# Performance work log

Hardware: AMD Instinct MI355X
Metric: run time of the kernel (lower is better)

## Reference

```python
import jax, jax.numpy as jnp
import numpy as np

N_NODES = 200000
N_EDGES = 1600000
N_GRAPHS = 2000
IN_DIM, W1_DIM, W2_DIM, N_CLASSES = 8, 64, 12, 2


def setup_inputs() -> dict:
    key = jax.random.key(0)
    ks = jax.random.split(key, 9)
    x = jax.random.normal(ks[0], (N_NODES, IN_DIM), dtype=jnp.float32)
    edge_index = jax.random.randint(ks[1], (2, N_EDGES), 0, N_NODES, dtype=jnp.int64)
    batch_index = jnp.sort(jax.random.randint(ks[2], (N_NODES,), 0, N_GRAPHS, dtype=jnp.int64))
    # Glorot-ish scaled params
    W1 = jax.random.normal(ks[3], (IN_DIM, W1_DIM), dtype=jnp.float32) * (1.0 / np.sqrt(IN_DIM))
    b1 = jnp.zeros((W1_DIM,), dtype=jnp.float32)
    W2 = jax.random.normal(ks[4], (W1_DIM, W2_DIM), dtype=jnp.float32) * (1.0 / np.sqrt(W1_DIM))
    b2 = jnp.zeros((W2_DIM,), dtype=jnp.float32)
    Wl = jax.random.normal(ks[5], (W2_DIM, N_CLASSES), dtype=jnp.float32) * (1.0 / np.sqrt(W2_DIM))
    bl = jnp.zeros((N_CLASSES,), dtype=jnp.float32)
    return {"x": x, "edge_index": edge_index, "batch_index": batch_index,
            "W1": W1, "b1": b1, "W2": W2, "b2": b2, "Wl": Wl, "bl": bl}


def _gcn_conv(x, W, b, src, dst, deg_inv_sqrt, n_nodes):
    # x' = D^{-1/2} (A + I) D^{-1/2} X W + b  (self-loops already in src/dst)
    xw = x @ W                                   # [N, out]
    norm = deg_inv_sqrt[src] * deg_inv_sqrt[dst]  # [E+N]
    msg = xw[src] * norm[:, None]                 # edge-wise gather (memory-bound)
    out = jax.ops.segment_sum(msg, dst, num_segments=n_nodes)
    return out + b


def reference(x, edge_index, batch_index, W1, b1, W2, b2, Wl, bl):
    n = x.shape[0]
    loops = jnp.arange(n, dtype=edge_index.dtype)
    src = jnp.concatenate([edge_index[0], loops])
    dst = jnp.concatenate([edge_index[1], loops])
    # degree (with self-loops) on destination nodes, as in PyG gcn_norm
    deg = jax.ops.segment_sum(jnp.ones_like(dst, dtype=x.dtype), dst, num_segments=n)
    deg_inv_sqrt = jax.lax.rsqrt(deg)  # deg >= 1 due to self-loops
    h = jax.nn.relu(_gcn_conv(x, W1, b1, src, dst, deg_inv_sqrt, n))
    h = jax.nn.relu(_gcn_conv(h, W2, b2, src, dst, deg_inv_sqrt, n))
    pooled = jax.ops.segment_max(h, batch_index, num_segments=N_GRAPHS)  # global_max_pool
    logits = pooled @ Wl + bl
    return jax.nn.log_softmax(logits, axis=1)
```

## Files before the change

### kernel.cpp

```cpp
#include <hip/hip_runtime.h>
#include <hip/hip_fp16.h>
#include <stdint.h>


constexpr int IN_DIM = 8;
constexpr int H1 = 64;
constexpr int H2 = 12;
constexpr int NPB = 512;
constexpr int NBK = 391;
constexpr int CAP = 4608;
constexpr int CHUNK = 4096;
constexpr int SLOTS = 16;

typedef float nfloat4 __attribute__((ext_vector_type(4)));
__device__ __forceinline__ void nt_store_f4(void* p, float4 v) {
    nfloat4 w = {v.x, v.y, v.z, v.w};
    __builtin_nontemporal_store(w, (nfloat4*)p);
}

__device__ __forceinline__ void acc_row8(float* acc, int4 rv) {
    const __half2* h = (const __half2*)&rv;
#pragma unroll
    for (int q = 0; q < 4; ++q) {
        float2 f = __half22float2(h[q]);
        acc[2 * q] += f.x; acc[2 * q + 1] += f.y;
    }
}

__global__ void k_binA(const int* __restrict__ src, const int* __restrict__ dst,
                       uint32_t* __restrict__ pairs, int* __restrict__ bcursor, int ne) {
    __shared__ int s_cur[NBK];
    __shared__ int s_gb[NBK];
    for (int i = threadIdx.x; i < NBK; i += 256) s_cur[i] = 0;
    __syncthreads();
    int e0 = blockIdx.x * CHUNK;
    int rec[16];
#pragma unroll
    for (int i = 0; i < 16; ++i) {
        int e = e0 + i * 256 + threadIdx.x;
        rec[i] = -1;
        if (e < ne) {
            int d = __builtin_nontemporal_load(&dst[e]);
            int b = d >> 9;
            int off = atomicAdd(&s_cur[b], 1);
            rec[i] = (off << 18) | ((d & 511) << 9) | b;
        }
    }
    __syncthreads();
    for (int b = threadIdx.x; b < NBK; b += 256) {
        int c = s_cur[b];
        s_gb[b] = (c > 0) ? atomicAdd(&bcursor[b], c) : 0;
    }
    __syncthreads();
#pragma unroll
    for (int i = 0; i < 16; ++i) {
        if (rec[i] < 0) continue;
        int e = e0 + i * 256 + threadIdx.x;
        int b = rec[i] & 511;
        int dl = (rec[i] >> 9) & 511;
        int off = (rec[i] >> 18) + s_gb[b];
        if (off < CAP)
            pairs[(size_t)b * CAP + off] =
                ((uint32_t)dl << 18) | (uint32_t)__builtin_nontemporal_load(&src[e]);
    }
}

__global__ void __launch_bounds__(256) k_binB(
        const uint32_t* __restrict__ pairs, const int* __restrict__ bcursor,
        const float* __restrict__ x, int* __restrict__ csr_pad,
        int* __restrict__ csr_ovf, unsigned int* __restrict__ meta,
        float* __restrict__ dis, __half2* __restrict__ xdh, int n) {
    __shared__ int s_hist[NPB];
    __shared__ int s_start[NPB];
    __shared__ int s_cur[NPB];
    __shared__ int s_tmp[256];
    __shared__ int s_pad[NPB * SLOTS];
    int b = blockIdx.x;
    int t = threadIdx.x;
    int cnt = min(bcursor[b], CAP);
    const uint32_t* pb = pairs + (size_t)b * CAP;
    for (int i = t; i < NPB; i += 256) { s_hist[i] = 0; s_cur[i] = 0; }
    for (int i = t; i < NPB * SLOTS; i += 256) s_pad[i] = n;
    __syncthreads();
    for (int i = t; i < cnt; i += 256)
        atomicAdd(&s_hist[__builtin_nontemporal_load(&pb[i]) >> 18], 1);
    __syncthreads();
    int b2i = t * 2;
    int v0 = s_hist[b2i], v1 = s_hist[b2i + 1];
    int tot = v0 + v1;
    s_tmp[t] = tot;
    __syncthreads();
    for (int off = 1; off < 256; off <<= 1) {
        int u = (t >= off) ? s_tmp[t - off] : 0;
        __syncthreads();
        s_tmp[t] += u;
        __syncthreads();
    }
    int ex = s_tmp[t] - tot;
    s_start[b2i] = ex;
    s_start[b2i + 1] = ex + v0;
    __syncthreads();
    int cb = b * CAP;
    int node0 = b << 9;
    for (int i = t; i < NPB; i += 256) {
        int node = node0 + i;
        if (node < n) {
            meta[node] = ((unsigned int)s_hist[i] << 21) | (unsigned int)(cb + s_start[i]);
            float di = rsqrtf((float)(s_hist[i] + 1));
            dis[node] = di;
            const float4* xi = (const float4*)(x + (size_t)node * IN_DIM);
            float4 a = xi[0], c = xi[1];
            union { __half2 h[4]; int iv[4]; } u;
            u.h[0] = __float22half2_rn(make_float2(a.x * di, a.y * di));
            u.h[1] = __float22half2_rn(make_float2(a.z * di, a.w * di));
            u.h[2] = __float22half2_rn(make_float2(c.x * di, c.y * di));
            u.h[3] = __float22half2_rn(make_float2(c.z * di, c.w * di));
            ((int4*)xdh)[node] = make_int4(u.iv[0], u.iv[1], u.iv[2], u.iv[3]);
        } else if (node == n) {
            ((int4*)xdh)[n] = make_int4(0, 0, 0, 0);
        }
    }
    __syncthreads();
    for (int i = t; i < cnt; i += 256) {
        uint32_t p = __builtin_nontemporal_load(&pb[i]);
        int dl = p >> 18;
        int sidx = (int)(p & 0x3FFFFu);
        int pos = atomicAdd(&s_cur[dl], 1);
        if (pos < SLOTS) s_pad[dl * SLOTS + pos] = sidx;
        else             csr_ovf[cb + s_start[dl] + pos] = sidx;
    }
    __syncthreads();
    for (int i = t; i < NPB * SLOTS / 4; i += 256) {
        int node = node0 + (i >> 2);
        if (node < n)
            ((int4*)csr_pad)[(size_t)node0 * 4 + i] = ((int4*)s_pad)[i];
    }
}

__global__ void __launch_bounds__(256) k_agg1f(
        const int* __restrict__ csr_pad, const int* __restrict__ csr_ovf,
        const unsigned int* __restrict__ meta, const __half2* __restrict__ xdh,
        const float* __restrict__ dis, const float* __restrict__ W1,
        const float* __restrict__ b1, const float* __restrict__ W2,
        __half2* __restrict__ y2h, int n) {
    __shared__ float sW1[IN_DIM * H1];
    __shared__ float sW2[H1 * H2];
    __shared__ float sb1[H1];
    for (int i = threadIdx.x; i < IN_DIM * H1; i += 256) sW1[i] = W1[i];
    for (int i = threadIdx.x; i < H1 * H2; i += 256) sW2[i] = W2[i];
    if (threadIdx.x < H1) sb1[threadIdx.x] = b1[threadIdx.x];
    __syncthreads();
    int node = blockIdx.x * 256 + threadIdx.x;
    if (node > n) return;
    int4* orow = (int4*)y2h + (size_t)node * 2;
    if (node == n) {
        orow[0] = make_int4(0, 0, 0, 0);
        orow[1] = make_int4(0, 0, 0, 0);
        return;
    }
    const int4* pr = (const int4*)(csr_pad + (size_t)node * SLOTS);
    int4 p0 = pr[0], p1 = pr[1], p2 = pr[2], p3 = pr[3];
    unsigned int m = meta[node];
    const int4* xt = (const int4*)xdh;

    float acc[8] = {0, 0, 0, 0, 0, 0, 0, 0};
    int idx[16] = {p0.x, p0.y, p0.z, p0.w, p1.x, p1.y, p1.z, p1.w,
                   p2.x, p2.y, p2.z, p2.w, p3.x, p3.y, p3.z, p3.w};
    acc_row8(acc, xt[node]);
#pragma unroll
    for (int i = 0; i < 16; ++i) acc_row8(acc, xt[(size_t)idx[i]]);
    int deg = m >> 21;
    if (deg > SLOTS) {
        int r0 = (int)(m & 0x1FFFFF);
        for (int r = SLOTS; r < deg; ++r) acc_row8(acc, xt[(size_t)csr_ovf[r0 + r]]);
    }
    float di = dis[node];
    float z[8];
#pragma unroll
    for (int k = 0; k < 8; ++k) z[k] = acc[k] * di;

    float y2[H2];
#pragma unroll
    for (int j = 0; j < H2; ++j) y2[j] = 0.f;
    for (int d = 0; d < H1; ++d) {
        float h = sb1[d];
#pragma unroll
        for (int k = 0; k < 8; ++k) h = fmaf(z[k], sW1[k * H1 + d], h);
        h = fmaxf(h, 0.f);
#pragma unroll
        for (int j = 0; j < H2; ++j) y2[j] = fmaf(h, sW2[d * H2 + j], y2[j]);
    }
    union { __half2 h2v[8]; int iv[8]; } u;
#pragma unroll
    for (int q = 0; q < 6; ++q)
        u.h2v[q] = __float22half2_rn(make_float2(y2[2 * q] * di, y2[2 * q + 1] * di));
    u.h2v[6] = __float22half2_rn(make_float2(0.f, 0.f));
    u.h2v[7] = u.h2v[6];
    orow[0] = make_int4(u.iv[0], u.iv[1], u.iv[2], u.iv[3]);
    orow[1] = make_int4(u.iv[4], u.iv[5], u.iv[6], u.iv[7]);
}

__global__ void __launch_bounds__(256) k_agg2(
        const int* __restrict__ csr_pad, const int* __restrict__ csr_ovf,
        const unsigned int* __restrict__ meta, const __half2* __restrict__ y2h,
        const float* __restrict__ dis, const float* __restrict__ b2,
        float* __restrict__ h2, int n) {
    int node = blockIdx.x * 256 + threadIdx.x;
    if (node >= n) return;
    const int4* pr = (const int4*)(csr_pad + (size_t)node * SLOTS);
    int4 p0 = pr[0], p1 = pr[1], p2 = pr[2], p3 = pr[3];
    unsigned int m = meta[node];
    const int4* yt = (const int4*)y2h;

    float acc[12] = {0, 0, 0, 0, 0, 0, 0, 0, 0, 0, 0, 0};
    auto addrow = [&](int nb) {
        int4 ra = yt[(size_t)nb * 2];
        int4 rb = yt[(size_t)nb * 2 + 1];
        const __half2* ha = (const __half2*)&ra;
        const __half2* hb = (const __half2*)&rb;
#pragma unroll
        for (int q = 0; q < 4; ++q) {
            float2 f = __half22float2(ha[q]);
            acc[2 * q] += f.x; acc[2 * q + 1] += f.y;
        }
#pragma unroll
        for (int q = 0; q < 2; ++q) {
            float2 f = __half22float2(hb[q]);
            acc[8 + 2 * q] += f.x; acc[9 + 2 * q] += f.y;
        }
    };
    int idx[16] = {p0.x, p0.y, p0.z, p0.w, p1.x, p1.y, p1.z, p1.w,
                   p2.x, p2.y, p2.z, p2.w, p3.x, p3.y, p3.z, p3.w};
    addrow(node);
#pragma unroll
    for (int i = 0; i < 16; ++i) addrow(idx[i]);
    int deg = m >> 21;
    if (deg > SLOTS) {
        int r0 = (int)(m & 0x1FFFFF);
        for (int r = SLOTS; r < deg; ++r) addrow(csr_ovf[r0 + r]);
    }
    float di = dis[node];
    float4 v0, v1, v2;
    v0.x = fmaxf(fmaf(acc[0], di, b2[0]), 0.f);
    v0.y = fmaxf(fmaf(acc[1], di, b2[1]), 0.f);
    v0.z = fmaxf(fmaf(acc[2], di, b2[2]), 0.f);
    v0.w = fmaxf(fmaf(acc[3], di, b2[3]), 0.f);
    v1.x = fmaxf(fmaf(acc[4], di, b2[4]), 0.f);
    v1.y = fmaxf(fmaf(acc[5], di, b2[5]), 0.f);
    v1.z = fmaxf(fmaf(acc[6], di, b2[6]), 0.f);
    v1.w = fmaxf(fmaf(acc[7], di, b2[7]), 0.f);
    v2.x = fmaxf(fmaf(acc[8], di, b2[8]), 0.f);
    v2.y = fmaxf(fmaf(acc[9], di, b2[9]), 0.f);
    v2.z = fmaxf(fmaf(acc[10], di, b2[10]), 0.f);
    v2.w = fmaxf(fmaf(acc[11], di, b2[11]), 0.f);
    float* o = h2 + (size_t)node * H2;
    nt_store_f4(o, v0);
    nt_store_f4(o + 4, v1);
    nt_store_f4(o + 8, v2);
}

__global__ void __launch_bounds__(128) k_pool(
        const float* __restrict__ h2, const int* __restrict__ batch,
        const float* __restrict__ Wl, const float* __restrict__ bl,
        float* __restrict__ out, int n) {
    __shared__ float s_m[120];
    __shared__ float s_p[12];
    __shared__ int s_be[2];
    int g = blockIdx.x;
    int t = threadIdx.x;
    if (t < 2) {
        int target = g + t;
        int lo = 0, hi = n;
        while (lo < hi) {
            int mid = (lo + hi) >> 1;
            if (batch[mid] < target) lo = mid + 1; else hi = mid;
        }
        s_be[t] = lo;
    }
    __syncthreads();
    int gs = s_be[0], ge = s_be[1];
    if (t < 120) {
        int off = t / 12, dim = t - off * 12;
        float m = 0.f;
        for (int i = gs + off; i < ge; i += 10)
            m = fmaxf(m, h2[(size_t)i * 12 + dim]);
        s_m[t] = m;
    }
    __syncthreads();
    if (t < 12) {
        float m = s_m[t];
#pragma unroll
        for (int k = 1; k < 10; ++k) m = fmaxf(m, s_m[t + 12 * k]);
        s_p[t] = m;
    }
    __syncthreads();
    if (t == 0) {
        float l0 = bl[0], l1 = bl[1];
#pragma unroll
        for (int k = 0; k < H2; ++k) {
            float pv = s_p[k];
            l0 = fmaf(pv, Wl[k * 2 + 0], l0);
            l1 = fmaf(pv, Wl[k * 2 + 1], l1);
        }
        float m = fmaxf(l0, l1);
        float lse = m + logf(expf(l0 - m) + expf(l1 - m));
        out[g * 2 + 0] = l0 - lse;
        out[g * 2 + 1] = l1 - lse;
    }
}

extern "C" void kernel_launch(void* const* d_in, const int* in_sizes, int n_in,
                              void* d_out, int out_size, void* d_ws, size_t ws_size,
                              hipStream_t stream) {
    const float* x   = (const float*)d_in[0];
    const int* ei    = (const int*)d_in[1];
    const int* batch = (const int*)d_in[2];
    const float* W1  = (const float*)d_in[3];
    const float* b1  = (const float*)d_in[4];
    const float* W2  = (const float*)d_in[5];
    const float* b2  = (const float*)d_in[6];
    const float* Wl  = (const float*)d_in[7];
    const float* bl  = (const float*)d_in[8];
    float* out = (float*)d_out;

    const int N = in_sizes[0] / IN_DIM;
    const int E = in_sizes[1] / 2;
    const int G = out_size / 2;
    const int* src = ei;
    const int* dst = ei + E;

    auto cdiv = [](long long a, int b) { return (int)((a + b - 1) / b); };

    char* wp = (char*)d_ws;
    auto carve = [&](size_t bytes) {
        char* p = wp;
        wp += (bytes + 63) & ~(size_t)63;
        return p;
    };
    int*          bcursor = (int*)carve(NBK * 4);
    unsigned int* meta    = (unsigned int*)carve((size_t)N * 4);
    float*        dis     = (float*)carve((size_t)N * 4);
    __half2*      xdh     = (__half2*)carve((size_t)(N + 1) * 16);
    __half2*      y2h     = (__half2*)carve((size_t)(N + 1) * 32);
    float*        h2      = (float*)carve((size_t)N * H2 * 4);
    uint32_t*     pairs   = (uint32_t*)carve((size_t)NBK * CAP * 4);
    int*          csr_pad = (int*)carve((size_t)N * SLOTS * 4);
    int*          csr_ovf = (int*)carve((size_t)NBK * CAP * 4);

    (void)hipMemsetAsync(bcursor, 0, NBK * sizeof(int), stream);

    k_binA<<<cdiv(E, CHUNK), 256, 0, stream>>>(src, dst, pairs, bcursor, E);
    k_binB<<<NBK, 256, 0, stream>>>(pairs, bcursor, x, csr_pad, csr_ovf,
                                    meta, dis, xdh, N);

    k_agg1f<<<cdiv((long long)N + 1, 256), 256, 0, stream>>>(
        csr_pad, csr_ovf, meta, xdh, dis, W1, b1, W2, y2h, N);
    k_agg2<<<cdiv(N, 256), 256, 0, stream>>>(csr_pad, csr_ovf, meta, y2h, dis, b2, h2, N);
    k_pool<<<G, 128, 0, stream>>>(h2, batch, Wl, bl, out, N);
}
```

Measured before the change: 192.7 us.

## Fuse max-pool into layer-2 aggregation and stage binning through shared memory

The global max pool moves into the layer-2 aggregation kernel. A wavefront segmented max scan over sorted batch ids is followed by atomicMax on float bits, so the h2 intermediate and the per-graph pool kernel go away and a small head kernel computes the logits. Binning changes to 256-node buckets. k_binA now scans its counts locally and stages records in shared memory, so global writes to the pairs array are contiguous per bucket. The uint atomicMax trick relies on values being non-negative after ReLU, with zero-initialized pooled buffers, and adds atomic traffic.

Result: faster. 175.2 us, median of 2 (-9.1%).

```diff
diff --git a/kernel.cpp b/kernel.cpp
--- a/kernel.cpp
+++ b/kernel.cpp
@@ -6,17 +6,11 @@
 constexpr int IN_DIM = 8;
 constexpr int H1 = 64;
 constexpr int H2 = 12;
-constexpr int NPB = 512;
-constexpr int NBK = 391;
-constexpr int CAP = 4608;
+constexpr int NPB = 256;
+constexpr int NBK = 782;
+constexpr int CAP = 2560;
 constexpr int CHUNK = 4096;
 constexpr int SLOTS = 16;
-
-typedef float nfloat4 __attribute__((ext_vector_type(4)));
-__device__ __forceinline__ void nt_store_f4(void* p, float4 v) {
-    nfloat4 w = {v.x, v.y, v.z, v.w};
-    __builtin_nontemporal_store(w, (nfloat4*)p);
-}
 
 __device__ __forceinline__ void acc_row8(float* acc, int4 rv) {
     const __half2* h = (const __half2*)&rv;
@@ -27,41 +21,73 @@
     }
 }
 
-__global__ void k_binA(const int* __restrict__ src, const int* __restrict__ dst,
-                       uint32_t* __restrict__ pairs, int* __restrict__ bcursor, int ne) {
-    __shared__ int s_cur[NBK];
+__global__ void __launch_bounds__(256) k_binA(
+        const int* __restrict__ src, const int* __restrict__ dst,
+        uint32_t* __restrict__ pairs, int* __restrict__ bcursor, int ne) {
+    __shared__ int s_cnt[NBK];
+    __shared__ int s_start[NBK];
     __shared__ int s_gb[NBK];
-    for (int i = threadIdx.x; i < NBK; i += 256) s_cur[i] = 0;
+    __shared__ int s_tmp[256];
+    __shared__ uint32_t s_img[CHUNK];
+    __shared__ uint16_t s_bkt[CHUNK];
+    int t = threadIdx.x;
+    for (int i = t; i < NBK; i += 256) s_cnt[i] = 0;
     __syncthreads();
     int e0 = blockIdx.x * CHUNK;
+    int cntblk = min(CHUNK, ne - e0);
     int rec[16];
 #pragma unroll
     for (int i = 0; i < 16; ++i) {
-        int e = e0 + i * 256 + threadIdx.x;
+        int e = e0 + i * 256 + t;
         rec[i] = -1;
         if (e < ne) {
             int d = __builtin_nontemporal_load(&dst[e]);
-            int b = d >> 9;
-            int off = atomicAdd(&s_cur[b], 1);
-            rec[i] = (off << 18) | ((d & 511) << 9) | b;
+            int b = d >> 8;
+            int off = atomicAdd(&s_cnt[b], 1);
+            rec[i] = (off << 18) | ((d & 255) << 10) | b;
         }
     }
     __syncthreads();
-    for (int b = threadIdx.x; b < NBK; b += 256) {
-        int c = s_cur[b];
+    int b4 = t * 4;
+    int v0 = (b4 < NBK) ? s_cnt[b4] : 0;
+    int v1 = (b4 + 1 < NBK) ? s_cnt[b4 + 1] : 0;
+    int v2 = (b4 + 2 < NBK) ? s_cnt[b4 + 2] : 0;
+    int v3 = (b4 + 3 < NBK) ? s_cnt[b4 + 3] : 0;
+    int p1 = v0, p2 = v0 + v1, p3 = v0 + v1 + v2, tot = p3 + v3;
+    s_tmp[t] = tot;
+    __syncthreads();
+    for (int off = 1; off < 256; off <<= 1) {
+        int u = (t >= off) ? s_tmp[t - off] : 0;
+        __syncthreads();
+        s_tmp[t] += u;
+        __syncthreads();
+    }
+    int ex = s_tmp[t] - tot;
+    if (b4 < NBK)     s_start[b4] = ex;
+    if (b4 + 1 < NBK) s_start[b4 + 1] = ex + p1;
+    if (b4 + 2 < NBK) s_start[b4 + 2] = ex + p2;
+    if (b4 + 3 < NBK) s_start[b4 + 3] = ex + p3;
+    for (int b = t; b < NBK; b += 256) {
+        int c = s_cnt[b];
         s_gb[b] = (c > 0) ? atomicAdd(&bcursor[b], c) : 0;
     }
     __syncthreads();
 #pragma unroll
     for (int i = 0; i < 16; ++i) {
         if (rec[i] < 0) continue;
-        int e = e0 + i * 256 + threadIdx.x;
-        int b = rec[i] & 511;
-        int dl = (rec[i] >> 9) & 511;
-        int off = (rec[i] >> 18) + s_gb[b];
-        if (off < CAP)
-            pairs[(size_t)b * CAP + off] =
-                ((uint32_t)dl << 18) | (uint32_t)__builtin_nontemporal_load(&src[e]);
+        int e = e0 + i * 256 + t;
+        int b = rec[i] & 1023;
+        int dl = (rec[i] >> 10) & 255;
+        int off = rec[i] >> 18;
+        int pos = s_start[b] + off;
+        s_img[pos] = ((uint32_t)dl << 18) | (uint32_t)__builtin_nontemporal_load(&src[e]);
+        s_bkt[pos] = (uint16_t)b;
+    }
+    __syncthreads();
+    for (int i = t; i < cntblk; i += 256) {
+        int b = s_bkt[i];
+        int goff = s_gb[b] + (i - s_start[b]);
+        if (goff < CAP) pairs[(size_t)b * CAP + goff] = s_img[i];
     }
 }
 
@@ -79,16 +105,14 @@
     int t = threadIdx.x;
     int cnt = min(bcursor[b], CAP);
     const uint32_t* pb = pairs + (size_t)b * CAP;
-    for (int i = t; i < NPB; i += 256) { s_hist[i] = 0; s_cur[i] = 0; }
+    s_hist[t] = 0; s_cur[t] = 0;
     for (int i = t; i < NPB * SLOTS; i += 256) s_pad[i] = n;
     __syncthreads();
     for (int i = t; i < cnt; i += 256)
         atomicAdd(&s_hist[__builtin_nontemporal_load(&pb[i]) >> 18], 1);
     __syncthreads();
-    int b2i = t * 2;
-    int v0 = s_hist[b2i], v1 = s_hist[b2i + 1];
-    int tot = v0 + v1;
-    s_tmp[t] = tot;
+    int v = s_hist[t];
+    s_tmp[t] = v;
     __syncthreads();
     for (int off = 1; off < 256; off <<= 1) {
         int u = (t >= off) ? s_tmp[t - off] : 0;
@@ -96,29 +120,25 @@
         s_tmp[t] += u;
         __syncthreads();
     }
-    int ex = s_tmp[t] - tot;
-    s_start[b2i] = ex;
-    s_start[b2i + 1] = ex + v0;
+    s_start[t] = s_tmp[t] - v;
     __syncthreads();
     int cb = b * CAP;
-    int node0 = b << 9;
-    for (int i = t; i < NPB; i += 256) {
-        int node = node0 + i;
-        if (node < n) {
-            meta[node] = ((unsigned int)s_hist[i] << 21) | (unsigned int)(cb + s_start[i]);
-            float di = rsqrtf((float)(s_hist[i] + 1));
-            dis[node] = di;
-            const float4* xi = (const float4*)(x + (size_t)node * IN_DIM);
-            float4 a = xi[0], c = xi[1];
-            union { __half2 h[4]; int iv[4]; } u;
-            u.h[0] = __float22half2_rn(make_float2(a.x * di, a.y * di));
-            u.h[1] = __float22half2_rn(make_float2(a.z * di, a.w * di));
-            u.h[2] = __float22half2_rn(make_float2(c.x * di, c.y * di));
-            u.h[3] = __float22half2_rn(make_float2(c.z * di, c.w * di));
-            ((int4*)xdh)[node] = make_int4(u.iv[0], u.iv[1], u.iv[2], u.iv[3]);
-        } else if (node == n) {
-            ((int4*)xdh)[n] = make_int4(0, 0, 0, 0);
-        }
+    int node = (b << 8) + t;
+    if (node < n) {
+        int deg = s_hist[t];
+        meta[node] = ((unsigned int)deg << 21) | (unsigned int)(cb + s_start[t]);
+        float di = rsqrtf((float)(deg + 1));
+        dis[node] = di;
+        const float4* xi = (const float4*)(x + (size_t)node * IN_DIM);
+        float4 a = xi[0], c = xi[1];
+        union { __half2 h[4]; int iv[4]; } u;
+        u.h[0] = __float22half2_rn(make_float2(a.x * di, a.y * di));
+        u.h[1] = __float22half2_rn(make_float2(a.z * di, a.w * di));
+        u.h[2] = __float22half2_rn(make_float2(c.x * di, c.y * di));
+        u.h[3] = __float22half2_rn(make_float2(c.z * di, c.w * di));
+        ((int4*)xdh)[node] = make_int4(u.iv[0], u.iv[1], u.iv[2], u.iv[3]);
+    } else if (node == n) {
+        ((int4*)xdh)[n] = make_int4(0, 0, 0, 0);
     }
     __syncthreads();
     for (int i = t; i < cnt; i += 256) {
@@ -131,9 +151,9 @@
     }
     __syncthreads();
     for (int i = t; i < NPB * SLOTS / 4; i += 256) {
-        int node = node0 + (i >> 2);
-        if (node < n)
-            ((int4*)csr_pad)[(size_t)node0 * 4 + i] = ((int4*)s_pad)[i];
+        int node2 = (b << 8) + (i >> 2);
+        if (node2 < n)
+            ((int4*)csr_pad)[(size_t)(b << 8) * 4 + i] = ((int4*)s_pad)[i];
     }
 }
 
@@ -204,109 +224,84 @@
         const int* __restrict__ csr_pad, const int* __restrict__ csr_ovf,
         const unsigned int* __restrict__ meta, const __half2* __restrict__ y2h,
         const float* __restrict__ dis, const float* __restrict__ b2,
-        float* __restrict__ h2, int n) {
+        const int* __restrict__ batch, unsigned int* __restrict__ pooled, int n) {
     int node = blockIdx.x * 256 + threadIdx.x;
-    if (node >= n) return;
-    const int4* pr = (const int4*)(csr_pad + (size_t)node * SLOTS);
-    int4 p0 = pr[0], p1 = pr[1], p2 = pr[2], p3 = pr[3];
-    unsigned int m = meta[node];
-    const int4* yt = (const int4*)y2h;
-
-    float acc[12] = {0, 0, 0, 0, 0, 0, 0, 0, 0, 0, 0, 0};
-    auto addrow = [&](int nb) {
-        int4 ra = yt[(size_t)nb * 2];
-        int4 rb = yt[(size_t)nb * 2 + 1];
-        const __half2* ha = (const __half2*)&ra;
-        const __half2* hb = (const __half2*)&rb;
-#pragma unroll
-        for (int q = 0; q < 4; ++q) {
-            float2 f = __half22float2(ha[q]);
-            acc[2 * q] += f.x; acc[2 * q + 1] += f.y;
+    int lane = threadIdx.x & 63;
+    bool active = node < n;
+    float v[12] = {0, 0, 0, 0, 0, 0, 0, 0, 0, 0, 0, 0};
+    int gid = 0x7fffffff;
+    if (active) {
+        const int4* pr = (const int4*)(csr_pad + (size_t)node * SLOTS);
+        int4 p0 = pr[0], p1 = pr[1], p2 = pr[2], p3 = pr[3];
+        unsigned int m = meta[node];
+        const int4* yt = (const int4*)y2h;
+        float acc[12] = {0, 0, 0, 0, 0, 0, 0, 0, 0, 0, 0, 0};
+        auto addrow = [&](int nb) {
+            int4 ra = yt[(size_t)nb * 2];
+            int4 rb = yt[(size_t)nb * 2 + 1];
+            const __half2* ha = (const __half2*)&ra;
+            const __half2* hb = (const __half2*)&rb;
+#pragma unroll
+            for (int q = 0; q < 4; ++q) {
+                float2 f = __half22float2(ha[q]);
+                acc[2 * q] += f.x; acc[2 * q + 1] += f.y;
+            }
+#pragma unroll
+            for (int q = 0; q < 2; ++q) {
+                float2 f = __half22float2(hb[q]);
+                acc[8 + 2 * q] += f.x; acc[9 + 2 * q] += f.y;
+            }
+        };
+        int idx[16] = {p0.x, p0.y, p0.z, p0.w, p1.x, p1.y, p1.z, p1.w,
+                       p2.x, p2.y, p2.z, p2.w, p3.x, p3.y, p3.z, p3.w};
+        addrow(node);
+#pragma unroll
+        for (int i = 0; i < 16; ++i) addrow(idx[i]);
+        int deg = m >> 21;
+        if (deg > SLOTS) {
+            int r0 = (int)(m & 0x1FFFFF);
+            for (int r = SLOTS; r < deg; ++r) addrow(csr_ovf[r0 + r]);
         }
-#pragma unroll
-        for (int q = 0; q < 2; ++q) {
-            float2 f = __half22float2(hb[q]);
-            acc[8 + 2 * q] += f.x; acc[9 + 2 * q] += f.y;
+        float di = dis[node];
+#pragma unroll
+        for (int q = 0; q < 12; ++q) v[q] = fmaxf(fmaf(acc[q], di, b2[q]), 0.f);
+        gid = batch[node];
+    }
+#pragma unroll
+    for (int off = 1; off < 64; off <<= 1) {
+        int g2 = __shfl_up(gid, off, 64);
+        bool merge = (lane >= off) && (g2 == gid);
+#pragma unroll
+        for (int q = 0; q < 12; ++q) {
+            float tv = __shfl_up(v[q], off, 64);
+            if (merge) v[q] = fmaxf(v[q], tv);
         }
-    };
-    int idx[16] = {p0.x, p0.y, p0.z, p0.w, p1.x, p1.y, p1.z, p1.w,
-                   p2.x, p2.y, p2.z, p2.w, p3.x, p3.y, p3.z, p3.w};
-    addrow(node);
-#pragma unroll
-    for (int i = 0; i < 16; ++i) addrow(idx[i]);
-    int deg = m >> 21;
-    if (deg > SLOTS) {
-        int r0 = (int)(m & 0x1FFFFF);
-        for (int r = SLOTS; r < deg; ++r) addrow(csr_ovf[r0 + r]);
-    }
-    float di = dis[node];
-    float4 v0, v1, v2;
-    v0.x = fmaxf(fmaf(acc[0], di, b2[0]), 0.f);
-    v0.y = fmaxf(fmaf(acc[1], di, b2[1]), 0.f);
-    v0.z = fmaxf(fmaf(acc[2], di, b2[2]), 0.f);
-    v0.w = fmaxf(fmaf(acc[3], di, b2[3]), 0.f);
-    v1.x = fmaxf(fmaf(acc[4], di, b2[4]), 0.f);
-    v1.y = fmaxf(fmaf(acc[5], di, b2[5]), 0.f);
-    v1.z = fmaxf(fmaf(acc[6], di, b2[6]), 0.f);
-    v1.w = fmaxf(fmaf(acc[7], di, b2[7]), 0.f);
-    v2.x = fmaxf(fmaf(acc[8], di, b2[8]), 0.f);
-    v2.y = fmaxf(fmaf(acc[9], di, b2[9]), 0.f);
-    v2.z = fmaxf(fmaf(acc[10], di, b2[10]), 0.f);
-    v2.w = fmaxf(fmaf(acc[11], di, b2[11]), 0.f);
-    float* o = h2 + (size_t)node * H2;
-    nt_store_f4(o, v0);
-    nt_store_f4(o + 4, v1);
-    nt_store_f4(o + 8, v2);
-}
-
-__global__ void __launch_bounds__(128) k_pool(
-        const float* __restrict__ h2, const int* __restrict__ batch,
-        const float* __restrict__ Wl, const float* __restrict__ bl,
-        float* __restrict__ out, int n) {
-    __shared__ float s_m[120];
-    __shared__ float s_p[12];
-    __shared__ int s_be[2];
-    int g = blockIdx.x;
-    int t = threadIdx.x;
-    if (t < 2) {
-        int target = g + t;
-        int lo = 0, hi = n;
-        while (lo < hi) {
-            int mid = (lo + hi) >> 1;
-            if (batch[mid] < target) lo = mid + 1; else hi = mid;
-        }
-        s_be[t] = lo;
-    }
-    __syncthreads();
-    int gs = s_be[0], ge = s_be[1];
-    if (t < 120) {
-        int off = t / 12, dim = t - off * 12;
-        float m = 0.f;
-        for (int i = gs + off; i < ge; i += 10)
-            m = fmaxf(m, h2[(size_t)i * 12 + dim]);
-        s_m[t] = m;
-    }
-    __syncthreads();
-    if (t < 12) {
-        float m = s_m[t];
-#pragma unroll
-        for (int k = 1; k < 10; ++k) m = fmaxf(m, s_m[t + 12 * k]);
-        s_p[t] = m;
-    }
-    __syncthreads();
-    if (t == 0) {
-        float l0 = bl[0], l1 = bl[1];
-#pragma unroll
-        for (int k = 0; k < H2; ++k) {
-            float pv = s_p[k];
-            l0 = fmaf(pv, Wl[k * 2 + 0], l0);
-            l1 = fmaf(pv, Wl[k * 2 + 1], l1);
-        }
-        float m = fmaxf(l0, l1);
-        float lse = m + logf(expf(l0 - m) + expf(l1 - m));
-        out[g * 2 + 0] = l0 - lse;
-        out[g * 2 + 1] = l1 - lse;
-    }
+    }
+    int gnext = __shfl_down(gid, 1, 64);
+    bool last = (lane == 63) || (gnext != gid);
+    if (last && gid != 0x7fffffff) {
+        unsigned int* pp = pooled + (size_t)gid * 12;
+#pragma unroll
+        for (int q = 0; q < 12; ++q) atomicMax(&pp[q], __float_as_uint(v[q]));
+    }
+}
+
+__global__ void k_head(const unsigned int* __restrict__ pooled,
+                       const float* __restrict__ Wl, const float* __restrict__ bl,
+                       float* __restrict__ out, int g) {
+    int i = blockIdx.x * 256 + threadIdx.x;
+    if (i >= g) return;
+    float l0 = bl[0], l1 = bl[1];
+#pragma unroll
+    for (int k = 0; k < H2; ++k) {
+        float pv = __uint_as_float(pooled[(size_t)i * 12 + k]);
+        l0 = fmaf(pv, Wl[k * 2 + 0], l0);
+        l1 = fmaf(pv, Wl[k * 2 + 1], l1);
+    }
+    float m = fmaxf(l0, l1);
+    float lse = m + logf(expf(l0 - m) + expf(l1 - m));
+    out[i * 2 + 0] = l0 - lse;
+    out[i * 2 + 1] = l1 - lse;
 }
 
 extern "C" void kernel_launch(void* const* d_in, const int* in_sizes, int n_in,
@@ -338,16 +333,17 @@
         return p;
     };
     int*          bcursor = (int*)carve(NBK * 4);
+    unsigned int* pooled  = (unsigned int*)carve((size_t)G * H2 * 4);
     unsigned int* meta    = (unsigned int*)carve((size_t)N * 4);
     float*        dis     = (float*)carve((size_t)N * 4);
     __half2*      xdh     = (__half2*)carve((size_t)(N + 1) * 16);
     __half2*      y2h     = (__half2*)carve((size_t)(N + 1) * 32);
-    float*        h2      = (float*)carve((size_t)N * H2 * 4);
     uint32_t*     pairs   = (uint32_t*)carve((size_t)NBK * CAP * 4);
     int*          csr_pad = (int*)carve((size_t)N * SLOTS * 4);
     int*          csr_ovf = (int*)carve((size_t)NBK * CAP * 4);
 
-    (void)hipMemsetAsync(bcursor, 0, NBK * sizeof(int), stream);
+    size_t zspan = (char*)(pooled + (size_t)G * H2) - (char*)bcursor;
+    (void)hipMemsetAsync(bcursor, 0, zspan, stream);
 
     k_binA<<<cdiv(E, CHUNK), 256, 0, stream>>>(src, dst, pairs, bcursor, E);
     k_binB<<<NBK, 256, 0, stream>>>(pairs, bcursor, x, csr_pad, csr_ovf,
@@ -355,6 +351,7 @@
 
     k_agg1f<<<cdiv((long long)N + 1, 256), 256, 0, stream>>>(
         csr_pad, csr_ovf, meta, xdh, dis, W1, b1, W2, y2h, N);
-    k_agg2<<<cdiv(N, 256), 256, 0, stream>>>(csr_pad, csr_ovf, meta, y2h, dis, b2, h2, N);
-    k_pool<<<G, 128, 0, stream>>>(h2, batch, Wl, bl, out, N);
-}
+    k_agg2<<<cdiv(N, 256), 256, 0, stream>>>(csr_pad, csr_ovf, meta, y2h, dis, b2,
+                                             batch, pooled, N);
+    k_head<<<cdiv(G, 256), 256, 0, stream>>>(pooled, Wl, bl, out, G);
+}
```
